# Kernel tuning notes

Hardware: AMD Instinct MI355X
Metric: run time of the kernel (lower is better)

## Reference

```python
import jax, jax.numpy as jnp
import numpy as np

# static config (mirrors init_kwargs)
F_T, S = 8, 24            # video_shape = (F_T, S, S)
K, DIL = 3, 1             # kernel_size, dilation (same for all 3 axes)
HEADS, DHEAD, DIM = 8, 64, 512
INNER = HEADS * DHEAD
PAD = DIL * (K - 1)       # causal: pad 2 at the FRONT of each spatial axis
KJ = K ** 3               # 27 neighbors per query
N_VID = F_T * S * S       # 4608 video tokens


def causal_pad(t):
    # t: [B, D, F, S, S] -> pad front of f/h/w axes (torch F.pad (PAD*?,0) causal layout)
    return jnp.pad(t, ((0, 0), (0, 0), (PAD, 0), (PAD, 0), (PAD, 0)))


def unfold3d(t):
    # torch unfoldNd equivalent. t: [B, D, F+PAD, S+PAD, S+PAD]
    # returns [B, N_VID, KJ, D]; kernel offsets ordered (kf, kh, kw) w fastest,
    # matching torch unfold's channel-major / kernel-minor layout after the
    # rearrange 'b (d j) i -> b i j d'.
    sl = []
    for i in range(K):
        for j in range(K):
            for kk in range(K):
                sl.append(t[:, :, i * DIL:i * DIL + F_T,
                                  j * DIL:j * DIL + S,
                                  kk * DIL:kk * DIL + S])
    u = jnp.stack(sl, axis=2)                      # [B, D, KJ, F, S, S]
    B, D = t.shape[0], t.shape[1]
    u = u.reshape(B, D, KJ, N_VID)
    return jnp.transpose(u, (0, 3, 2, 1))          # [B, N_VID, KJ, D]


def make_mask():
    # True where the neighbor falls into zero padding (out-of-range / future under causal pad)
    ones = jnp.ones((1, 1, F_T, S, S), jnp.float32)
    u = unfold3d(causal_pad(ones))[0, :, :, 0]     # [N_VID, KJ]
    m = u == 0.0
    return jnp.pad(m, ((0, 0), (1, 0)), constant_values=False)  # bos col never masked


def stable_softmax(t, alpha=32.0 ** 2):
    t = t / alpha
    t = t - jax.lax.stop_gradient(jnp.max(t, axis=-1, keepdims=True))
    return jax.nn.softmax(t * alpha, axis=-1)


def setup_inputs() -> dict:
    key = jax.random.key(0)
    ks = jax.random.split(key, 9)
    return {
        "x": jax.random.normal(ks[0], (1, N_VID + 1, DIM), jnp.float32),
        "Wq": jax.random.normal(ks[1], (DIM, INNER), jnp.float32) * 0.02,
        "Wkv": jax.random.normal(ks[2], (DIM, 2 * INNER), jnp.float32) * 0.02,
        "W_th": jax.random.normal(ks[3], (HEADS, HEADS), jnp.float32) * 0.2,
        "Wout": jax.random.normal(ks[4], (INNER, DIM), jnp.float32) * 0.02,
        "bout": jax.random.normal(ks[5], (DIM,), jnp.float32) * 0.02,
        "ax1": jax.random.normal(ks[6], (K, HEADS), jnp.float32),
        "ax2": jax.random.normal(ks[7], (K, HEADS), jnp.float32),
        "ax3": jax.random.normal(ks[8], (K, HEADS), jnp.float32),
    }


def reference(x, Wq, Wkv, W_th, Wout, bout, ax1, ax2, ax3):
    b, n, _ = x.shape                       # b=1, n = 1 + N_VID (no extra padding)
    h, d = HEADS, DHEAD
    scale = d ** -0.5

    q = x @ Wq
    k, v = jnp.split(x @ Wkv, 2, axis=-1)

    def to_heads(t):  # 'b n (h d) -> (b h) n d'
        return t.reshape(b, n, h, d).transpose(0, 2, 1, 3).reshape(b * h, n, d)

    q, k, v = map(to_heads, (q, k, v))
    q = q[:, 1:] * scale                    # drop bos query
    k_bos, v_bos = k[:, :1], v[:, :1]       # [bh, 1, d]
    k, v = k[:, 1:], v[:, 1:]

    def to_vid(t):  # 'b (f h w) d -> b d f h w'
        return t.reshape(b * h, F_T, S, S, d).transpose(0, 4, 1, 2, 3)

    ku = unfold3d(causal_pad(to_vid(k)))    # [bh, N, KJ, d]
    vu = unfold3d(causal_pad(to_vid(v)))
    N = ku.shape[1]

    kb = jnp.broadcast_to(k_bos[:, :, None, :], (b * h, N, 1, d))
    vb = jnp.broadcast_to(v_bos[:, :, None, :], (b * h, N, 1, d))
    ku = jnp.concatenate([kb, ku], axis=2)  # [bh, N, KJ+1, d]
    vu = jnp.concatenate([vb, vu], axis=2)

    sim = jnp.einsum('bid,bijd->bij', q, ku)                 # [bh, N, KJ+1]

    # axial relative position bias over the 3x3x3 kernel, pad 0 for bos column
    rel = (ax1[:, None, None, :] + ax2[None, :, None, :] + ax3[None, None, :, :])
    rel = rel.reshape(KJ, h)                                 # [27, h]
    bias = jnp.pad(rel.T[:, None, :], ((0, 0), (0, 0), (1, 0)))  # [h, 1, KJ+1]

    sim = sim.reshape(b, h, N, KJ + 1) + bias[None]
    mask = make_mask()                                       # [N, KJ+1]
    sim = jnp.where(mask[None, None], -jnp.finfo(sim.dtype).max, sim)

    attn = stable_softmax(sim)                               # [b, h, N, KJ+1]
    attn = jnp.einsum('hg,bgij->bhij', W_th, attn)           # talking heads 1x1 conv

    out = jnp.einsum('bhij,bhijd->bhid', attn, vu.reshape(b, h, N, KJ + 1, d))
    out = jnp.concatenate([v_bos.reshape(b, h, 1, d), out], axis=2)  # re-attach bos value
    out = out.transpose(0, 2, 1, 3).reshape(b, n, h * d)     # '(b h) n d -> b n (h d)'
    return out @ Wout + bout
```

## Files before the change

### kernel.cpp

```cpp
#include <hip/hip_runtime.h>
#include <hip/hip_bf16.h>


constexpr int TFR   = 8;
constexpr int SDIM  = 24;
constexpr int NVID  = TFR * SDIM * SDIM;
constexpr int NTOK  = NVID + 1;
constexpr int NH    = 8;
constexpr int DM    = 512;
constexpr int NJ    = 28;

typedef __attribute__((ext_vector_type(8))) short bf16x8;
typedef __attribute__((ext_vector_type(8))) unsigned short ushort8;
typedef __attribute__((ext_vector_type(4))) float f32x4;

typedef const __attribute__((address_space(1))) unsigned int* gas_ptr;
typedef __attribute__((address_space(3))) unsigned int* las_ptr;

__device__ __forceinline__ float bf2f(unsigned short u) {
    return __uint_as_float((unsigned)u << 16);
}

constexpr int CAST_BLOCKS = (NTOK * DM / 4 + 255) / 256;

__global__ __launch_bounds__(256)
void prep_kernel(const float* __restrict__ x,
                 const float* __restrict__ Wq, const float* __restrict__ Wkv,
                 const float* __restrict__ Wout,
                 __hip_bfloat16* __restrict__ Xb,
                 __hip_bfloat16* __restrict__ Wqkvt,
                 __hip_bfloat16* __restrict__ Woutt)
{
    const int b   = blockIdx.x;
    const int tid = threadIdx.x;

    if (b < CAST_BLOCKS) {
        const int i = (b * 256 + tid) * 4;
        if (i >= NTOK * DM) return;
        const float4 v = *(const float4*)(x + i);
        Xb[i + 0] = __float2bfloat16(v.x);
        Xb[i + 1] = __float2bfloat16(v.y);
        Xb[i + 2] = __float2bfloat16(v.z);
        Xb[i + 3] = __float2bfloat16(v.w);
        return;
    }

    __shared__ float t[32][33];
    int tb = b - CAST_BLOCKS;
    const float* W; __hip_bfloat16* Wt; int Nd, tX, rowOff;
    if (tb < 256)      { W = Wq;   Wt = Wqkvt; Nd = 512;  tX = 16; rowOff = 0;   }
    else if (tb < 768) { tb -= 256; W = Wkv;  Wt = Wqkvt; Nd = 1024; tX = 32; rowOff = 512; }
    else               { tb -= 768; W = Wout; Wt = Woutt; Nd = 512;  tX = 16; rowOff = 0;   }
    const int n0 = (tb % tX) * 32, k0 = (tb / tX) * 32;
    const int r  = tid >> 3;
    const int c4 = (tid & 7) * 4;
    const float4 v = *(const float4*)(W + (size_t)(k0 + r) * Nd + n0 + c4);
    t[r][c4 + 0] = v.x; t[r][c4 + 1] = v.y; t[r][c4 + 2] = v.z; t[r][c4 + 3] = v.w;
    __syncthreads();
    #pragma unroll
    for (int j = 0; j < 4; ++j)
        Wt[(size_t)(rowOff + n0 + r) * 512 + k0 + c4 + j] = __float2bfloat16(t[c4 + j][r]);
}

template<int BM, int BN, int AM, int AN, int MODE>
__global__ __launch_bounds__(256)
void gemm_mfma(const __hip_bfloat16* __restrict__ A,
               const __hip_bfloat16* __restrict__ Bt,
               float* __restrict__ C, __hip_bfloat16* __restrict__ Cb,
               int M, int N, int K, const float* __restrict__ bias)
{
    constexpr int BK = 64;
    __shared__ __align__(16) short As[BM * BK];
    __shared__ __align__(16) short Bs[BN * BK];

    const int tid  = threadIdx.x;
    const int m0   = blockIdx.x * BM;
    const int n0   = blockIdx.y * BN;
    const int lane = tid & 63;
    const int wave = tid >> 6;
    const int wm   = (wave >> 1) * (AM * 16);
    const int wn   = (wave & 1) * (AN * 16);
    const int col  = lane & 15;
    const int quad = lane >> 4;

    f32x4 acc[AM][AN] = {};

    for (int k0 = 0; k0 < K; k0 += BK) {
        #pragma unroll
        for (int it = 0; it < BM * 8 / 256; ++it) {
            const int idx = it * 256 + tid;
            const int r   = idx >> 3;
            const int u   = (idx & 7) ^ (r & 7);
            const __hip_bfloat16* gp = A + (size_t)(m0 + r) * K + k0 + u * 8;
            __builtin_amdgcn_global_load_lds(
                (gas_ptr)gp, (las_ptr)&As[(it * 256 + wave * 64) * 8], 16, 0, 0);
        }
        #pragma unroll
        for (int it = 0; it < BN * 8 / 256; ++it) {
            const int idx = it * 256 + tid;
            const int r   = idx >> 3;
            const int u   = (idx & 7) ^ (r & 7);
            const __hip_bfloat16* gp = Bt + (size_t)(n0 + r) * K + k0 + u * 8;
            __builtin_amdgcn_global_load_lds(
                (gas_ptr)gp, (las_ptr)&Bs[(it * 256 + wave * 64) * 8], 16, 0, 0);
        }
        __syncthreads();

        #pragma unroll
        for (int ks = 0; ks < 2; ++ks) {
            bf16x8 af[AM], bfr[AN];
            #pragma unroll
            for (int mt = 0; mt < AM; ++mt) {
                const int r = wm + mt * 16 + col;
                const int u = (ks * 4 + quad) ^ (r & 7);
                af[mt] = *(const bf16x8*)(&As[r * BK + u * 8]);
            }
            #pragma unroll
            for (int nt = 0; nt < AN; ++nt) {
                const int r = wn + nt * 16 + col;
                const int u = (ks * 4 + quad) ^ (r & 7);
                bfr[nt] = *(const bf16x8*)(&Bs[r * BK + u * 8]);
            }
            #pragma unroll
            for (int mt = 0; mt < AM; ++mt)
                #pragma unroll
                for (int nt = 0; nt < AN; ++nt)
                    acc[mt][nt] = __builtin_amdgcn_mfma_f32_16x16x32_bf16(
                        af[mt], bfr[nt], acc[mt][nt], 0, 0, 0);
        }
        __syncthreads();
    }

    const bool isQ = (MODE == 1) && (n0 < 512);
    #pragma unroll
    for (int mt = 0; mt < AM; ++mt) {
        #pragma unroll
        for (int r = 0; r < 4; ++r) {
            const int row = m0 + wm + mt * 16 + quad * 4 + r;
            if (row >= M) continue;
            #pragma unroll
            for (int nt = 0; nt < AN; ++nt) {
                const int cg = n0 + wn + nt * 16 + col;
                float v = acc[mt][nt][r];
                if (MODE == 0) {
                    if (bias) v += bias[cg];
                    C[(size_t)row * N + cg] = v;
                } else if (isQ) {
                    C[(size_t)row * 512 + cg] = v;
                } else {
                    Cb[(size_t)row * 1024 + (cg - 512)] = __float2bfloat16(v);
                }
            }
        }
    }
}

__global__ __launch_bounds__(256)
void attn_v2(const float* __restrict__ Q, const __hip_bfloat16* __restrict__ KVb,
             __hip_bfloat16* __restrict__ O,
             const float* __restrict__ W_th,
             const float* __restrict__ ax1, const float* __restrict__ ax2,
             const float* __restrict__ ax3)
{
    __shared__ float attn_s[4][NH * NJ];
    __shared__ float mixed_s[4][NH * NJ];

    const int tid  = threadIdx.x;
    const int wave = tid >> 6;
    const int lane = tid & 63;
    const int g    = lane >> 3;
    const int s    = lane & 7;
    const int i    = __builtin_amdgcn_readfirstlane(blockIdx.x * 4 + (tid >> 6));
    const int qrow = i + 1;

    const int t  = i / (SDIM * SDIM);
    const int rm = i % (SDIM * SDIM);
    const int y  = rm / SDIM;
    const int x  = rm % SDIM;

    float qf[8];
    {
        const float4 q0 = *(const float4*)(Q + (size_t)qrow * DM + lane * 8);
        const float4 q1 = *(const float4*)(Q + (size_t)qrow * DM + lane * 8 + 4);
        qf[0] = q0.x * 0.125f; qf[1] = q0.y * 0.125f; qf[2] = q0.z * 0.125f; qf[3] = q0.w * 0.125f;
        qf[4] = q1.x * 0.125f; qf[5] = q1.y * 0.125f; qf[6] = q1.z * 0.125f; qf[7] = q1.w * 0.125f;
    }
    float a1[3], a2[3], a3[3];
    #pragma unroll
    for (int d = 0; d < 3; ++d) {
        a1[d] = ax1[d * NH + g];
        a2[d] = ax2[d * NH + g];
        a3[d] = ax3[d * NH + g];
    }

    float sim[NJ];
    #pragma unroll
    for (int j = 0; j < NJ; ++j) {
        int row; bool valid; float bias;
        if (j == 0) { row = 0; valid = true; bias = 0.f; }
        else {
            const int jp = j - 1;
            const int di = jp / 9, dj = (jp / 3) % 3, dk = jp % 3;
            const int tt = t + di - 2, yy = y + dj - 2, xx = x + dk - 2;
            valid = (tt >= 0) && (yy >= 0) && (xx >= 0);
            row = 1 + tt * SDIM * SDIM + yy * SDIM + xx;
            bias = a1[di] + a2[dj] + a3[dk];
        }
        if (valid) {
            const ushort8 kv = *(const ushort8*)(KVb + (size_t)row * 1024 + lane * 8);
            float p = 0.f;
            #pragma unroll
            for (int e = 0; e < 8; ++e) p += bf2f(kv[e]) * qf[e];
            p += __shfl_xor(p, 1);
            p += __shfl_xor(p, 2);
            p += __shfl_xor(p, 4);
            sim[j] = p + bias;
        } else {
            sim[j] = -1e30f;
        }
    }

    float m = -1e30f;
    #pragma unroll
    for (int j = 0; j < NJ; ++j) m = fmaxf(m, sim[j]);
    float ssum = 0.f;
    #pragma unroll
    for (int j = 0; j < NJ; ++j) { sim[j] = __expf(sim[j] - m); ssum += sim[j]; }
    const float inv = 1.f / ssum;
    #pragma unroll
    for (int j = 0; j < NJ; ++j) sim[j] *= inv;

    if (s == 0) {
        #pragma unroll
        for (int u = 0; u < 7; ++u) {
            f32x4 v4 = { sim[4*u], sim[4*u+1], sim[4*u+2], sim[4*u+3] };
            *(f32x4*)(&attn_s[wave][g * NJ + 4 * u]) = v4;
        }
    }
    __syncthreads();

    if (tid < NH * NJ) {
        const int h = tid / NJ, j = tid % NJ;
        #pragma unroll
        for (int q = 0; q < 4; ++q) {
            float acc = 0.f;
            #pragma unroll
            for (int gg = 0; gg < NH; ++gg)
                acc += W_th[h * NH + gg] * attn_s[q][gg * NJ + j];
            mixed_s[q][h * NJ + j] = acc;
        }
    }
    __syncthreads();

    float acc8[8] = {};
    #pragma unroll
    for (int j = 0; j < NJ; ++j) {
        int row; bool valid;
        if (j == 0) { row = 0; valid = true; }
        else {
            const int jp = j - 1;
            const int di = jp / 9, dj = (jp / 3) % 3, dk = jp % 3;
            const int tt = t + di - 2, yy = y + dj - 2, xx = x + dk - 2;
            valid = (tt >= 0) && (yy >= 0) && (xx >= 0);
            row = 1 + tt * SDIM * SDIM + yy * SDIM + xx;
        }
        if (valid) {
            const ushort8 vv = *(const ushort8*)(KVb + (size_t)row * 1024 + 512 + lane * 8);
            const float w = mixed_s[wave][g * NJ + j];
            #pragma unroll
            for (int e = 0; e < 8; ++e) acc8[e] += w * bf2f(vv[e]);
        }
    }

    __hip_bfloat16 o[8];
    #pragma unroll
    for (int e = 0; e < 8; ++e) o[e] = __float2bfloat16(acc8[e]);
    *(ushort8*)(O + (size_t)qrow * DM + lane * 8) = *(const ushort8*)o;

    if (i == 0) {
        const ushort8 vb = *(const ushort8*)(KVb + 512 + lane * 8);
        *(ushort8*)(O + lane * 8) = vb;
    }
}

extern "C" void kernel_launch(void* const* d_in, const int* in_sizes, int n_in,
                              void* d_out, int out_size, void* d_ws, size_t ws_size,
                              hipStream_t stream)
{
    const float* x    = (const float*)d_in[0];
    const float* Wq   = (const float*)d_in[1];
    const float* Wkv  = (const float*)d_in[2];
    const float* W_th = (const float*)d_in[3];
    const float* Wout = (const float*)d_in[4];
    const float* bout = (const float*)d_in[5];
    const float* ax1  = (const float*)d_in[6];
    const float* ax2  = (const float*)d_in[7];
    const float* ax3  = (const float*)d_in[8];
    float* out = (float*)d_out;

    char* p = (char*)d_ws;
    float* Qf = (float*)p;                         p += (size_t)NTOK * DM * 4;
    __hip_bfloat16* KVb   = (__hip_bfloat16*)p;    p += (size_t)NTOK * 2 * DM * 2;
    __hip_bfloat16* Xb    = (__hip_bfloat16*)p;    p += (size_t)NTOK * DM * 2;
    __hip_bfloat16* Ob    = (__hip_bfloat16*)p;    p += (size_t)NTOK * DM * 2;
    __hip_bfloat16* Wqkvt = (__hip_bfloat16*)p;    p += (size_t)3 * DM * DM * 2;
    __hip_bfloat16* Woutt = (__hip_bfloat16*)p;    p += (size_t)DM * DM * 2;

    const dim3 blk(256);
    const int mtiles = (NTOK + 127) / 128;

    prep_kernel<<<CAST_BLOCKS + 1024, blk, 0, stream>>>(x, Wq, Wkv, Wout, Xb, Wqkvt, Woutt);

    gemm_mfma<128, 128, 4, 4, 1><<<dim3(mtiles, 12), blk, 0, stream>>>(
        Xb, Wqkvt, Qf, KVb, NTOK, 3 * DM, DM, nullptr);

    attn_v2<<<dim3(NVID / 4), blk, 0, stream>>>(Qf, KVb, Ob, W_th, ax1, ax2, ax3);

    gemm_mfma<128, 64, 4, 2, 0><<<dim3(mtiles, 8), blk, 0, stream>>>(
        Ob, Woutt, out, nullptr, NTOK, DM, DM, bout);
}
```

Before: 140.2 us.

## Fuse x bf16 cast into QKV GEMM, shrink output GEMM tiles, fold q scale

```diff
diff --git a/kernel.cpp b/kernel.cpp
--- a/kernel.cpp
+++ b/kernel.cpp
@@ -20,33 +20,19 @@
 __device__ __forceinline__ float bf2f(unsigned short u) {
     return __uint_as_float((unsigned)u << 16);
 }
-
-constexpr int CAST_BLOCKS = (NTOK * DM / 4 + 255) / 256;
+__device__ __forceinline__ unsigned short f2bf(float f) {
+    __hip_bfloat16 h = __float2bfloat16(f);
+    return reinterpret_cast<unsigned short&>(h);
+}
 
 __global__ __launch_bounds__(256)
-void prep_kernel(const float* __restrict__ x,
-                 const float* __restrict__ Wq, const float* __restrict__ Wkv,
-                 const float* __restrict__ Wout,
-                 __hip_bfloat16* __restrict__ Xb,
-                 __hip_bfloat16* __restrict__ Wqkvt,
-                 __hip_bfloat16* __restrict__ Woutt)
-{
-    const int b   = blockIdx.x;
+void prep_w(const float* __restrict__ Wq, const float* __restrict__ Wkv,
+            const float* __restrict__ Wout,
+            __hip_bfloat16* __restrict__ Wqkvt, __hip_bfloat16* __restrict__ Woutt)
+{
+    __shared__ float t[32][33];
     const int tid = threadIdx.x;
-
-    if (b < CAST_BLOCKS) {
-        const int i = (b * 256 + tid) * 4;
-        if (i >= NTOK * DM) return;
-        const float4 v = *(const float4*)(x + i);
-        Xb[i + 0] = __float2bfloat16(v.x);
-        Xb[i + 1] = __float2bfloat16(v.y);
-        Xb[i + 2] = __float2bfloat16(v.z);
-        Xb[i + 3] = __float2bfloat16(v.w);
-        return;
-    }
-
-    __shared__ float t[32][33];
-    int tb = b - CAST_BLOCKS;
+    int tb = blockIdx.x;
     const float* W; __hip_bfloat16* Wt; int Nd, tX, rowOff;
     if (tb < 256)      { W = Wq;   Wt = Wqkvt; Nd = 512;  tX = 16; rowOff = 0;   }
     else if (tb < 768) { tb -= 256; W = Wkv;  Wt = Wqkvt; Nd = 1024; tX = 32; rowOff = 512; }
@@ -62,15 +48,12 @@
         Wt[(size_t)(rowOff + n0 + r) * 512 + k0 + c4 + j] = __float2bfloat16(t[c4 + j][r]);
 }
 
-template<int BM, int BN, int AM, int AN, int MODE>
 __global__ __launch_bounds__(256)
-void gemm_mfma(const __hip_bfloat16* __restrict__ A,
-               const __hip_bfloat16* __restrict__ Bt,
-               float* __restrict__ C, __hip_bfloat16* __restrict__ Cb,
-               int M, int N, int K, const float* __restrict__ bias)
-{
-    constexpr int BK = 64;
-    __shared__ __align__(16) short As[BM * BK];
+void gemm_qkv(const float* __restrict__ A, const __hip_bfloat16* __restrict__ Bt,
+              float* __restrict__ Cq, __hip_bfloat16* __restrict__ Ckv, int M)
+{
+    constexpr int BM = 128, BN = 128, BK = 64, PITCH = 72, K = 512;
+    __shared__ short As[BM * PITCH];
     __shared__ __align__(16) short Bs[BN * BK];
 
     const int tid  = threadIdx.x;
@@ -78,16 +61,99 @@
     const int n0   = blockIdx.y * BN;
     const int lane = tid & 63;
     const int wave = tid >> 6;
-    const int wm   = (wave >> 1) * (AM * 16);
-    const int wn   = (wave & 1) * (AN * 16);
+    const int wm   = (wave >> 1) * 64;
+    const int wn   = (wave & 1) * 64;
     const int col  = lane & 15;
     const int quad = lane >> 4;
 
-    f32x4 acc[AM][AN] = {};
+    f32x4 acc[4][4] = {};
 
     for (int k0 = 0; k0 < K; k0 += BK) {
         #pragma unroll
-        for (int it = 0; it < BM * 8 / 256; ++it) {
+        for (int it = 0; it < 4; ++it) {
+            const int idx = it * 256 + tid;
+            const int r   = idx >> 3;
+            const int u   = (idx & 7) ^ (r & 7);
+            const __hip_bfloat16* gp = Bt + (size_t)(n0 + r) * K + k0 + u * 8;
+            __builtin_amdgcn_global_load_lds(
+                (gas_ptr)gp, (las_ptr)&Bs[(it * 256 + wave * 64) * 8], 16, 0, 0);
+        }
+        #pragma unroll
+        for (int r = 0; r < 4; ++r) {
+            const int m  = (tid >> 3) + r * 32;
+            const int k8 = (tid & 7) * 8;
+            const int gm = (m0 + m < M) ? (m0 + m) : (M - 1);
+            const float4 f0 = *(const float4*)(A + (size_t)gm * K + k0 + k8);
+            const float4 f1 = *(const float4*)(A + (size_t)gm * K + k0 + k8 + 4);
+            unsigned short v[8] = { f2bf(f0.x), f2bf(f0.y), f2bf(f0.z), f2bf(f0.w),
+                                    f2bf(f1.x), f2bf(f1.y), f2bf(f1.z), f2bf(f1.w) };
+            *(ushort8*)(&As[m * PITCH + k8]) = *(const ushort8*)v;
+        }
+        __syncthreads();
+
+        #pragma unroll
+        for (int ks = 0; ks < 2; ++ks) {
+            bf16x8 af[4], bfr[4];
+            #pragma unroll
+            for (int mt = 0; mt < 4; ++mt)
+                af[mt] = *(const bf16x8*)(&As[(wm + mt * 16 + col) * PITCH + ks * 32 + quad * 8]);
+            #pragma unroll
+            for (int nt = 0; nt < 4; ++nt) {
+                const int r = wn + nt * 16 + col;
+                const int u = (ks * 4 + quad) ^ (r & 7);
+                bfr[nt] = *(const bf16x8*)(&Bs[r * BK + u * 8]);
+            }
+            #pragma unroll
+            for (int mt = 0; mt < 4; ++mt)
+                #pragma unroll
+                for (int nt = 0; nt < 4; ++nt)
+                    acc[mt][nt] = __builtin_amdgcn_mfma_f32_16x16x32_bf16(
+                        af[mt], bfr[nt], acc[mt][nt], 0, 0, 0);
+        }
+        __syncthreads();
+    }
+
+    const bool isQ = (n0 < 512);
+    #pragma unroll
+    for (int mt = 0; mt < 4; ++mt) {
+        #pragma unroll
+        for (int r = 0; r < 4; ++r) {
+            const int row = m0 + wm + mt * 16 + quad * 4 + r;
+            if (row >= M) continue;
+            #pragma unroll
+            for (int nt = 0; nt < 4; ++nt) {
+                const int cg = n0 + wn + nt * 16 + col;
+                const float v = acc[mt][nt][r];
+                if (isQ) Cq[(size_t)row * 512 + cg] = v * 0.125f;
+                else     Ckv[(size_t)row * 1024 + (cg - 512)] = __float2bfloat16(v);
+            }
+        }
+    }
+}
+
+__global__ __launch_bounds__(256)
+void gemm_out(const __hip_bfloat16* __restrict__ A, const __hip_bfloat16* __restrict__ Bt,
+              float* __restrict__ C, int M, const float* __restrict__ bias)
+{
+    constexpr int BM = 64, BN = 64, BK = 64, K = 512;
+    __shared__ __align__(16) short As[BM * BK];
+    __shared__ __align__(16) short Bs[BN * BK];
+
+    const int tid  = threadIdx.x;
+    const int m0   = blockIdx.x * BM;
+    const int n0   = blockIdx.y * BN;
+    const int lane = tid & 63;
+    const int wave = tid >> 6;
+    const int wm   = (wave >> 1) * 32;
+    const int wn   = (wave & 1) * 32;
+    const int col  = lane & 15;
+    const int quad = lane >> 4;
+
+    f32x4 acc[2][2] = {};
+
+    for (int k0 = 0; k0 < K; k0 += BK) {
+        #pragma unroll
+        for (int it = 0; it < 2; ++it) {
             const int idx = it * 256 + tid;
             const int r   = idx >> 3;
             const int u   = (idx & 7) ^ (r & 7);
@@ -96,7 +162,7 @@
                 (gas_ptr)gp, (las_ptr)&As[(it * 256 + wave * 64) * 8], 16, 0, 0);
         }
         #pragma unroll
-        for (int it = 0; it < BN * 8 / 256; ++it) {
+        for (int it = 0; it < 2; ++it) {
             const int idx = it * 256 + tid;
             const int r   = idx >> 3;
             const int u   = (idx & 7) ^ (r & 7);
@@ -108,48 +174,39 @@
 
         #pragma unroll
         for (int ks = 0; ks < 2; ++ks) {
-            bf16x8 af[AM], bfr[AN];
-            #pragma unroll
-            for (int mt = 0; mt < AM; ++mt) {
+            bf16x8 af[2], bfr[2];
+            #pragma unroll
+            for (int mt = 0; mt < 2; ++mt) {
                 const int r = wm + mt * 16 + col;
                 const int u = (ks * 4 + quad) ^ (r & 7);
                 af[mt] = *(const bf16x8*)(&As[r * BK + u * 8]);
             }
             #pragma unroll
-            for (int nt = 0; nt < AN; ++nt) {
+            for (int nt = 0; nt < 2; ++nt) {
                 const int r = wn + nt * 16 + col;
                 const int u = (ks * 4 + quad) ^ (r & 7);
                 bfr[nt] = *(const bf16x8*)(&Bs[r * BK + u * 8]);
             }
             #pragma unroll
-            for (int mt = 0; mt < AM; ++mt)
+            for (int mt = 0; mt < 2; ++mt)
                 #pragma unroll
-                for (int nt = 0; nt < AN; ++nt)
+                for (int nt = 0; nt < 2; ++nt)
                     acc[mt][nt] = __builtin_amdgcn_mfma_f32_16x16x32_bf16(
                         af[mt], bfr[nt], acc[mt][nt], 0, 0, 0);
         }
         __syncthreads();
     }
 
-    const bool isQ = (MODE == 1) && (n0 < 512);
-    #pragma unroll
-    for (int mt = 0; mt < AM; ++mt) {
+    #pragma unroll
+    for (int mt = 0; mt < 2; ++mt) {
         #pragma unroll
         for (int r = 0; r < 4; ++r) {
             const int row = m0 + wm + mt * 16 + quad * 4 + r;
             if (row >= M) continue;
             #pragma unroll
-            for (int nt = 0; nt < AN; ++nt) {
+            for (int nt = 0; nt < 2; ++nt) {
                 const int cg = n0 + wn + nt * 16 + col;
-                float v = acc[mt][nt][r];
-                if (MODE == 0) {
-                    if (bias) v += bias[cg];
-                    C[(size_t)row * N + cg] = v;
-                } else if (isQ) {
-                    C[(size_t)row * 512 + cg] = v;
-                } else {
-                    Cb[(size_t)row * 1024 + (cg - 512)] = __float2bfloat16(v);
-                }
+                C[(size_t)row * 512 + cg] = acc[mt][nt][r] + bias[cg];
             }
         }
     }
@@ -182,8 +239,8 @@
     {
         const float4 q0 = *(const float4*)(Q + (size_t)qrow * DM + lane * 8);
         const float4 q1 = *(const float4*)(Q + (size_t)qrow * DM + lane * 8 + 4);
-        qf[0] = q0.x * 0.125f; qf[1] = q0.y * 0.125f; qf[2] = q0.z * 0.125f; qf[3] = q0.w * 0.125f;
-        qf[4] = q1.x * 0.125f; qf[5] = q1.y * 0.125f; qf[6] = q1.z * 0.125f; qf[7] = q1.w * 0.125f;
+        qf[0] = q0.x; qf[1] = q0.y; qf[2] = q0.z; qf[3] = q0.w;
+        qf[4] = q1.x; qf[5] = q1.y; qf[6] = q1.z; qf[7] = q1.w;
     }
     float a1[3], a2[3], a3[3];
     #pragma unroll
@@ -272,9 +329,9 @@
         }
     }
 
-    __hip_bfloat16 o[8];
-    #pragma unroll
-    for (int e = 0; e < 8; ++e) o[e] = __float2bfloat16(acc8[e]);
+    unsigned short o[8];
+    #pragma unroll
+    for (int e = 0; e < 8; ++e) o[e] = f2bf(acc8[e]);
     *(ushort8*)(O + (size_t)qrow * DM + lane * 8) = *(const ushort8*)o;
 
     if (i == 0) {
@@ -299,23 +356,21 @@
     float* out = (float*)d_out;
 
     char* p = (char*)d_ws;
-    float* Qf = (float*)p;                         p += (size_t)NTOK * DM * 4;
-    __hip_bfloat16* KVb   = (__hip_bfloat16*)p;    p += (size_t)NTOK * 2 * DM * 2;
-    __hip_bfloat16* Xb    = (__hip_bfloat16*)p;    p += (size_t)NTOK * DM * 2;
-    __hip_bfloat16* Ob    = (__hip_bfloat16*)p;    p += (size_t)NTOK * DM * 2;
-    __hip_bfloat16* Wqkvt = (__hip_bfloat16*)p;    p += (size_t)3 * DM * DM * 2;
-    __hip_bfloat16* Woutt = (__hip_bfloat16*)p;    p += (size_t)DM * DM * 2;
+    float* Qf = (float*)p;                       p += (size_t)NTOK * DM * 4;
+    __hip_bfloat16* KVb   = (__hip_bfloat16*)p;  p += (size_t)NTOK * 2 * DM * 2;
+    __hip_bfloat16* Ob    = (__hip_bfloat16*)p;  p += (size_t)NTOK * DM * 2;
+    __hip_bfloat16* Wqkvt = (__hip_bfloat16*)p;  p += (size_t)3 * DM * DM * 2;
+    __hip_bfloat16* Woutt = (__hip_bfloat16*)p;  p += (size_t)DM * DM * 2;
 
     const dim3 blk(256);
-    const int mtiles = (NTOK + 127) / 128;
-
-    prep_kernel<<<CAST_BLOCKS + 1024, blk, 0, stream>>>(x, Wq, Wkv, Wout, Xb, Wqkvt, Woutt);
-
-    gemm_mfma<128, 128, 4, 4, 1><<<dim3(mtiles, 12), blk, 0, stream>>>(
-        Xb, Wqkvt, Qf, KVb, NTOK, 3 * DM, DM, nullptr);
+    const int mtiles128 = (NTOK + 127) / 128;
+    const int mtiles64  = (NTOK + 63) / 64;
+
+    prep_w<<<1024, blk, 0, stream>>>(Wq, Wkv, Wout, Wqkvt, Woutt);
+
+    gemm_qkv<<<dim3(mtiles128, 12), blk, 0, stream>>>(x, Wqkvt, Qf, KVb, NTOK);
 
     attn_v2<<<dim3(NVID / 4), blk, 0, stream>>>(Qf, KVb, Ob, W_th, ax1, ax2, ax3);
 
-    gemm_mfma<128, 64, 4, 2, 0><<<dim3(mtiles, 8), blk, 0, stream>>>(
-        Ob, Woutt, out, nullptr, NTOK, DM, DM, bout);
-}
+    gemm_out<<<dim3(mtiles64, 8), blk, 0, stream>>>(Ob, Woutt, out, NTOK, bout);
+}
```

After: 134.0 us, median of 2. 4.4% less time.
